# Kernel optimization log

Measured on AMD Instinct MI355X. Metric: run time of the kernel, lower is better.

## Reference

```python
import jax, jax.numpy as jnp
import numpy as np


def setup_inputs() -> dict:
    key = jax.random.key(0)
    ks = jax.random.split(key, 9)
    B, C, H, W = 16, 64, 64, 64
    s = 0.02
    return {
        "x": jax.random.normal(ks[0], (B, C, H, W), dtype=jnp.float32),
        "qw": jax.random.normal(ks[1], (C, C), dtype=jnp.float32) * s,
        "qb": jax.random.normal(ks[2], (C,), dtype=jnp.float32) * s,
        "kw": jax.random.normal(ks[3], (C, C), dtype=jnp.float32) * s,
        "kb": jax.random.normal(ks[4], (C,), dtype=jnp.float32) * s,
        "vw": jax.random.normal(ks[5], (C, C), dtype=jnp.float32) * s,
        "vb": jax.random.normal(ks[6], (C,), dtype=jnp.float32) * s,
        "ow": jax.random.normal(ks[7], (C, C), dtype=jnp.float32) * s,
        "ob": jax.random.normal(ks[8], (C,), dtype=jnp.float32) * s,
    }


def reference(x, qw, qb, kw, kb, vw, vb, ow, ob):
    # x: [B, C, H, W]; 1x1 convs == per-pixel linear maps with weight [out_ch, in_ch]
    B, C, H, W = x.shape
    S = H * W
    xt = x.reshape(B, C, S).transpose(0, 2, 1)  # [B, S, C] tokens over spatial positions
    Q = jnp.einsum("bsc,oc->bso", xt, qw) + qb
    K = jnp.einsum("bsc,oc->bso", xt, kw) + kb
    V = jnp.einsum("bsc,oc->bso", xt, vw) + vb
    scale = 1.0 / jnp.sqrt(jnp.asarray(C, dtype=x.dtype))
    scores = jnp.einsum("bqc,bkc->bqk", Q, K) * scale  # [B, S, S]
    attn = jax.nn.softmax(scores, axis=-1)
    out = jnp.einsum("bqk,bkc->bqc", attn, V)  # [B, S, C]
    out = jnp.einsum("bsc,oc->bso", out, ow) + ob  # out 1x1 conv
    return out.transpose(0, 2, 1).reshape(B, C, H, W)
```

## Files before the change

kernel.cpp:

```cpp
#include <hip/hip_runtime.h>
#include <stdint.h>

#define SS 4096
#define CC 64
#define BB 16

typedef unsigned short u16;
typedef __attribute__((ext_vector_type(8))) __bf16 bf16x8;
typedef __attribute__((ext_vector_type(8))) short short8;
typedef __attribute__((ext_vector_type(4))) short s16x4;
typedef __attribute__((ext_vector_type(4))) float f32x4;

__device__ __forceinline__ uint32_t pkbf(float a, float b) {
    uint32_t ua = __float_as_uint(a) + 0x8000u;
    uint32_t ub = __float_as_uint(b) + 0x8000u;
    return __builtin_amdgcn_perm(ub, ua, 0x07060302u);
}

__device__ __forceinline__ uint32_t cvtpk(float a, float b) {
    uint32_t r;
    asm("v_cvt_pk_bf16_f32 %0, %1, %2" : "=v"(r) : "v"(a), "v"(b));
    return r;
}

__device__ __forceinline__ bf16x8 ldw8(const float* p) {
    f32x4 lo = *(const f32x4*)(p);
    f32x4 hi = *(const f32x4*)(p + 4);
    union { uint32_t u[4]; bf16x8 v; } r;
    r.u[0] = pkbf(lo[0], lo[1]);
    r.u[1] = pkbf(lo[2], lo[3]);
    r.u[2] = pkbf(hi[0], hi[1]);
    r.u[3] = pkbf(hi[2], hi[3]);
    return r.v;
}

__global__ __launch_bounds__(256, 4) void qkv_kernel(
    const float* __restrict__ x,
    const float* __restrict__ qw, const float* __restrict__ qb,
    const float* __restrict__ kw, const float* __restrict__ kb,
    const float* __restrict__ vw, const float* __restrict__ vb,
    u16* __restrict__ Q, u16* __restrict__ K, u16* __restrict__ VT)
{
    const int b    = blockIdx.x & 15;
    const int s0   = (blockIdx.x >> 4) << 6;
    const int tid  = threadIdx.x;
    const int w    = tid >> 6;
    const int lane = tid & 63;
    const int lq   = lane & 15;
    const int quad = lane >> 4;

    __shared__ u16 wt[3][64 * 72];
    __shared__ u16 xt[64 * 72];

    for (int m = 0; m < 3; ++m) {
        const float* wsrc = (m == 0) ? qw : ((m == 1) ? kw : vw);
#pragma unroll
        for (int i = 0; i < 8; ++i) {
            int p  = tid + (i << 8);
            int o  = p >> 5;
            int cp = p & 31;
            const float* wp = wsrc + o * 64 + cp * 2;
            ((uint32_t*)&wt[m][o * 72])[cp] = pkbf(wp[0], wp[1]);
        }
    }
    {
        const int sl = tid & 63;
        const int g  = tid >> 6;
        const float* xp = x + (size_t)b * CC * SS + s0 + sl;
#pragma unroll
        for (int i = 0; i < 8; ++i) {
            int p = g + (i << 2);
            float f0 = xp[(size_t)(2 * p) * SS];
            float f1 = xp[(size_t)(2 * p + 1) * SS];
            ((uint32_t*)&xt[sl * 72])[p] = pkbf(f0, f1);
        }
    }
    __syncthreads();

    bf16x8 a0 = *(const bf16x8*)&xt[(w * 16 + lq) * 72 + quad * 8];
    bf16x8 a1 = *(const bf16x8*)&xt[(w * 16 + lq) * 72 + 32 + quad * 8];
    __syncthreads();

    u16* bb = xt + w * (16 * 72);

    const float QSCALE = 0.125f * 1.44269504088896340736f;

    for (int m = 0; m < 3; ++m) {
        const float* bsrc = (m == 0) ? qb : ((m == 1) ? kb : vb);
        bf16x8 bfr[2][4];
#pragma unroll
        for (int kc = 0; kc < 2; ++kc)
#pragma unroll
            for (int nt = 0; nt < 4; ++nt)
                bfr[kc][nt] = *(const bf16x8*)&wt[m][(nt * 16 + lq) * 72 + kc * 32 + quad * 8];

        f32x4 acc[4];
#pragma unroll
        for (int nt = 0; nt < 4; ++nt) {
            float bv = bsrc[nt * 16 + lq];
            acc[nt] = (f32x4){bv, bv, bv, bv};
        }
#pragma unroll
        for (int nt = 0; nt < 4; ++nt) {
            acc[nt] = __builtin_amdgcn_mfma_f32_16x16x32_bf16(a0, bfr[0][nt], acc[nt], 0, 0, 0);
            acc[nt] = __builtin_amdgcn_mfma_f32_16x16x32_bf16(a1, bfr[1][nt], acc[nt], 0, 0, 0);
        }

        if (m == 2) {
#pragma unroll
            for (int nt = 0; nt < 4; ++nt) {
                int c = nt * 16 + lq;
                uint2 pv;
                pv.x = pkbf(acc[nt][0], acc[nt][1]);
                pv.y = pkbf(acc[nt][2], acc[nt][3]);
                *(uint2*)(VT + ((size_t)(b * CC + c)) * SS + s0 + w * 16 + quad * 4) = pv;
            }
        } else {
            const float scl = (m == 0) ? QSCALE : 1.0f;
#pragma unroll
            for (int nt = 0; nt < 4; ++nt)
#pragma unroll
                for (int r = 0; r < 4; ++r)
                    bb[(quad * 4 + r) * 72 + nt * 16 + lq] =
                        (u16)((__float_as_uint(acc[nt][r] * scl) + 0x8000u) >> 16);

            const int row = lane >> 2;
            const int ch  = (lane & 3) << 4;
            short8 v0 = *(const short8*)&bb[row * 72 + ch];
            short8 v1 = *(const short8*)&bb[row * 72 + ch + 8];
            u16* dst = ((m == 0) ? Q : K) + ((size_t)(b * SS + s0 + w * 16 + row)) * CC + ch;
            *(short8*)dst = v0;
            *(short8*)(dst + 8) = v1;
        }
    }
}

__global__ __launch_bounds__(256, 2) void flash_kernel(
    const u16* __restrict__ Q, const u16* __restrict__ K,
    const u16* __restrict__ Vt, const float* __restrict__ ow,
    const float* __restrict__ ob, float* __restrict__ out)
{
    const int b    = blockIdx.x & 15;
    const int q0   = (blockIdx.x >> 4) << 7;
    const int tid  = threadIdx.x;
    const int w    = tid >> 6;
    const int lane = tid & 63;
    const int lq   = lane & 15;
    const int quad = lane >> 4;

    __shared__ u16 lds_k[2][64 * 64];
    __shared__ u16 lds_v[2][64 * 64];
    __shared__ u16 lds_p[8][16 * 64];

    bf16x8 qf[2][2];
#pragma unroll
    for (int g = 0; g < 2; ++g) {
        const u16* qp = Q + ((size_t)(b * SS + q0 + g * 64 + w * 16 + lq)) * CC + quad * 8;
        qf[g][0] = *(const bf16x8*)(qp);
        qf[g][1] = *(const bf16x8*)(qp + 32);
    }

    f32x4 ot[2][4];
#pragma unroll
    for (int g = 0; g < 2; ++g)
#pragma unroll
        for (int ct = 0; ct < 4; ++ct) ot[g][ct] = (f32x4){0.f, 0.f, 0.f, 0.f};
    float lp[2][4] = {{0.f, 0.f, 0.f, 0.f}, {0.f, 0.f, 0.f, 0.f}};

    const f32x4 ZV = (f32x4){0.f, 0.f, 0.f, 0.f};

    const int srow = tid >> 2;
    const int a    = tid & 3;
    const u16* kg = K + ((size_t)(b * SS + srow)) * CC + a * 16;
    const u16* vg = Vt + ((size_t)(b * CC + srow)) * SS + a * 16;
    const int ssw = srow & 7;
    const int sw0 = srow * 64 + ((((a << 1)    ) ^ ssw) << 3);
    const int sw1 = srow * 64 + ((((a << 1) | 1) ^ ssw) << 3);
    const int kcs = (a >> 1) << 2;
    const int us  = (a & 1) << 2;
    const int vw0 = srow * 64 + (((kcs + 0) ^ ssw) << 3) + us;
    const int vw1 = srow * 64 + (((kcs + 1) ^ ssw) << 3) + us;
    const int vw2 = srow * 64 + (((kcs + 2) ^ ssw) << 3) + us;
    const int vw3 = srow * 64 + (((kcs + 3) ^ ssw) << 3) + us;

    {
        short8 k0 = *(const short8*)(kg);
        short8 k1 = *(const short8*)(kg + 8);
        union { short8 v; s16x4 h[2]; } v0, v1;
        v0.v = *(const short8*)(vg);
        v1.v = *(const short8*)(vg + 8);
        *(short8*)&lds_k[0][sw0] = k0;
        *(short8*)&lds_k[0][sw1] = k1;
        *(s16x4*)&lds_v[0][vw0] = v0.h[0];
        *(s16x4*)&lds_v[0][vw1] = v0.h[1];
        *(s16x4*)&lds_v[0][vw2] = v1.h[0];
        *(s16x4*)&lds_v[0][vw3] = v1.h[1];
    }

    const int lsw = lq & 7;
    u16* pw0 = lds_p[(w << 1)];
    u16* pw1 = lds_p[(w << 1) | 1];

    for (int kt = 0; kt < 64; ++kt) {
        __syncthreads();
        const int buf = kt & 1;

        const int ktn = (kt + 1) & 63;
        const u16* kgn = kg + (size_t)ktn * (64 * CC);
        const u16* vgn = vg + ktn * 64;
        short8 nk0 = *(const short8*)(kgn);
        short8 nk1 = *(const short8*)(kgn + 8);
        union { short8 v; s16x4 h[2]; } nv0, nv1;
        nv0.v = *(const short8*)(vgn);
        nv1.v = *(const short8*)(vgn + 8);

        bf16x8 kf[2][4];
#pragma unroll
        for (int kc = 0; kc < 2; ++kc)
#pragma unroll
            for (int mt = 0; mt < 4; ++mt)
                kf[kc][mt] = *(const bf16x8*)
                    &lds_k[buf][(mt * 16 + lq) * 64 + (((kc << 2) + quad) ^ lsw) * 8];

        f32x4 sa[2][4];
        __builtin_amdgcn_s_setprio(1);
#pragma unroll
        for (int g = 0; g < 2; ++g)
#pragma unroll
            for (int mt = 0; mt < 4; ++mt) {
                sa[g][mt] = __builtin_amdgcn_mfma_f32_16x16x32_bf16(
                    kf[0][mt], qf[g][0], ZV, 0, 0, 0);
                sa[g][mt] = __builtin_amdgcn_mfma_f32_16x16x32_bf16(
                    kf[1][mt], qf[g][1], sa[g][mt], 0, 0, 0);
            }
        __builtin_amdgcn_s_setprio(0);

        bf16x8 vf[2][4];
#pragma unroll
        for (int kc = 0; kc < 2; ++kc)
#pragma unroll
            for (int ct = 0; ct < 4; ++ct)
                vf[kc][ct] = *(const bf16x8*)
                    &lds_v[buf][(ct * 16 + lq) * 64 + (((kc << 2) + quad) ^ lsw) * 8];

#pragma unroll
        for (int g = 0; g < 2; ++g) {
            union { uint32_t u[4]; bf16x8 v; } pf[2];
#pragma unroll
            for (int mt = 0; mt < 4; ++mt) {
                float p0 = __builtin_amdgcn_exp2f(sa[g][mt][0]);
                float p1 = __builtin_amdgcn_exp2f(sa[g][mt][1]);
                float p2 = __builtin_amdgcn_exp2f(sa[g][mt][2]);
                float p3 = __builtin_amdgcn_exp2f(sa[g][mt][3]);
                lp[g][0] += p0; lp[g][1] += p1; lp[g][2] += p2; lp[g][3] += p3;
                pf[mt >> 1].u[(mt & 1) * 2 + 0] = cvtpk(p0, p1);
                pf[mt >> 1].u[(mt & 1) * 2 + 1] = cvtpk(p2, p3);
            }
            __builtin_amdgcn_s_setprio(1);
#pragma unroll
            for (int kc = 0; kc < 2; ++kc)
#pragma unroll
                for (int ct = 0; ct < 4; ++ct)
                    ot[g][ct] = __builtin_amdgcn_mfma_f32_16x16x32_bf16(
                        vf[kc][ct], pf[kc].v, ot[g][ct], 0, 0, 0);
            __builtin_amdgcn_s_setprio(0);
        }

        u16* lkd = lds_k[buf ^ 1];
        u16* lvd = lds_v[buf ^ 1];
        *(short8*)&lkd[sw0] = nk0;
        *(short8*)&lkd[sw1] = nk1;
        *(s16x4*)&lvd[vw0] = nv0.h[0];
        *(s16x4*)&lvd[vw1] = nv0.h[1];
        *(s16x4*)&lvd[vw2] = nv1.h[0];
        *(s16x4*)&lvd[vw3] = nv1.h[1];
    }

    bf16x8 wf[2][4];
#pragma unroll
    for (int kc = 0; kc < 2; ++kc)
#pragma unroll
        for (int nt = 0; nt < 4; ++nt)
            wf[kc][nt] = ldw8(ow + (nt * 16 + lq) * 64 + kc * 32 + quad * 8);
    float bias[4];
#pragma unroll
    for (int nt = 0; nt < 4; ++nt) bias[nt] = ob[nt * 16 + lq];

#pragma unroll
    for (int g = 0; g < 2; ++g) {
        float l = (lp[g][0] + lp[g][1]) + (lp[g][2] + lp[g][3]);
        l += __shfl_xor(l, 16);
        l += __shfl_xor(l, 32);
        const float inv = 1.0f / l;

        u16* po = g ? pw1 : pw0;
#pragma unroll
        for (int ct = 0; ct < 4; ++ct) {
            uint2 pv;
            pv.x = pkbf(ot[g][ct][0] * inv, ot[g][ct][1] * inv);
            pv.y = pkbf(ot[g][ct][2] * inv, ot[g][ct][3] * inv);
            *(uint2*)&po[lq * 64 + (((ct * 2 + (quad >> 1)) ^ lsw) << 3) + (quad & 1) * 4] = pv;
        }
        bf16x8 oa0 = *(const bf16x8*)&po[lq * 64 + (((0 * 4 + quad) ^ lsw) << 3)];
        bf16x8 oa1 = *(const bf16x8*)&po[lq * 64 + (((1 * 4 + quad) ^ lsw) << 3)];

        f32x4 acc[4];
#pragma unroll
        for (int nt = 0; nt < 4; ++nt)
            acc[nt] = (f32x4){bias[nt], bias[nt], bias[nt], bias[nt]};
#pragma unroll
        for (int nt = 0; nt < 4; ++nt) {
            acc[nt] = __builtin_amdgcn_mfma_f32_16x16x32_bf16(oa0, wf[0][nt], acc[nt], 0, 0, 0);
            acc[nt] = __builtin_amdgcn_mfma_f32_16x16x32_bf16(oa1, wf[1][nt], acc[nt], 0, 0, 0);
        }
#pragma unroll
        for (int nt = 0; nt < 4; ++nt) {
            float* dst = out + ((size_t)(b * CC + nt * 16 + lq)) * SS
                       + q0 + g * 64 + w * 16 + quad * 4;
            *(f32x4*)dst = acc[nt];
        }
    }
}

extern "C" void kernel_launch(void* const* d_in, const int* in_sizes, int n_in,
                              void* d_out, int out_size, void* d_ws, size_t ws_size,
                              hipStream_t stream)
{
    const float* x  = (const float*)d_in[0];
    const float* qw = (const float*)d_in[1];
    const float* qb = (const float*)d_in[2];
    const float* kw = (const float*)d_in[3];
    const float* kb = (const float*)d_in[4];
    const float* vw = (const float*)d_in[5];
    const float* vb = (const float*)d_in[6];
    const float* ow = (const float*)d_in[7];
    const float* ob = (const float*)d_in[8];
    float* out = (float*)d_out;

    const size_t T = (size_t)BB * SS * CC;
    u16* Q  = (u16*)d_ws;
    u16* K  = Q + T;
    u16* VT = K + T;

    qkv_kernel<<<dim3(BB * 64), dim3(256), 0, stream>>>(x, qw, qb, kw, kb, vw, vb, Q, K, VT);
    flash_kernel<<<dim3(BB * 32), dim3(256), 0, stream>>>(Q, K, VT, ow, ob, out);
}
```

Measured before the change: 163.1 us.

## Double query rows per flash block and interleave QK and PV per group

```diff
diff --git a/kernel.cpp b/kernel.cpp
--- a/kernel.cpp
+++ b/kernel.cpp
@@ -135,13 +135,13 @@
     }
 }
 
-__global__ __launch_bounds__(256, 2) void flash_kernel(
+__global__ __launch_bounds__(256, 1) void flash_kernel(
     const u16* __restrict__ Q, const u16* __restrict__ K,
     const u16* __restrict__ Vt, const float* __restrict__ ow,
     const float* __restrict__ ob, float* __restrict__ out)
 {
     const int b    = blockIdx.x & 15;
-    const int q0   = (blockIdx.x >> 4) << 7;
+    const int q0   = (blockIdx.x >> 4) << 8;
     const int tid  = threadIdx.x;
     const int w    = tid >> 6;
     const int lane = tid & 63;
@@ -150,22 +150,26 @@
 
     __shared__ u16 lds_k[2][64 * 64];
     __shared__ u16 lds_v[2][64 * 64];
-    __shared__ u16 lds_p[8][16 * 64];
-
-    bf16x8 qf[2][2];
-#pragma unroll
-    for (int g = 0; g < 2; ++g) {
-        const u16* qp = Q + ((size_t)(b * SS + q0 + g * 64 + w * 16 + lq)) * CC + quad * 8;
+    __shared__ u16 lds_p[4][1024];
+
+    bf16x8 qf[4][2];
+#pragma unroll
+    for (int g = 0; g < 4; ++g) {
+        const u16* qp = Q + ((size_t)(b * SS + q0 + w * 64 + g * 16 + lq)) * CC + quad * 8;
         qf[g][0] = *(const bf16x8*)(qp);
         qf[g][1] = *(const bf16x8*)(qp + 32);
     }
 
-    f32x4 ot[2][4];
-#pragma unroll
-    for (int g = 0; g < 2; ++g)
+    f32x4 ot[4][4];
+#pragma unroll
+    for (int g = 0; g < 4; ++g)
 #pragma unroll
         for (int ct = 0; ct < 4; ++ct) ot[g][ct] = (f32x4){0.f, 0.f, 0.f, 0.f};
-    float lp[2][4] = {{0.f, 0.f, 0.f, 0.f}, {0.f, 0.f, 0.f, 0.f}};
+    float lp[4][4];
+#pragma unroll
+    for (int g = 0; g < 4; ++g)
+#pragma unroll
+        for (int r = 0; r < 4; ++r) lp[g][r] = 0.f;
 
     const f32x4 ZV = (f32x4){0.f, 0.f, 0.f, 0.f};
 
@@ -198,8 +202,6 @@
     }
 
     const int lsw = lq & 7;
-    u16* pw0 = lds_p[(w << 1)];
-    u16* pw1 = lds_p[(w << 1) | 1];
 
     for (int kt = 0; kt < 64; ++kt) {
         __syncthreads();
@@ -221,20 +223,6 @@
             for (int mt = 0; mt < 4; ++mt)
                 kf[kc][mt] = *(const bf16x8*)
                     &lds_k[buf][(mt * 16 + lq) * 64 + (((kc << 2) + quad) ^ lsw) * 8];
-
-        f32x4 sa[2][4];
-        __builtin_amdgcn_s_setprio(1);
-#pragma unroll
-        for (int g = 0; g < 2; ++g)
-#pragma unroll
-            for (int mt = 0; mt < 4; ++mt) {
-                sa[g][mt] = __builtin_amdgcn_mfma_f32_16x16x32_bf16(
-                    kf[0][mt], qf[g][0], ZV, 0, 0, 0);
-                sa[g][mt] = __builtin_amdgcn_mfma_f32_16x16x32_bf16(
-                    kf[1][mt], qf[g][1], sa[g][mt], 0, 0, 0);
-            }
-        __builtin_amdgcn_s_setprio(0);
-
         bf16x8 vf[2][4];
 #pragma unroll
         for (int kc = 0; kc < 2; ++kc)
@@ -244,18 +232,30 @@
                     &lds_v[buf][(ct * 16 + lq) * 64 + (((kc << 2) + quad) ^ lsw) * 8];
 
 #pragma unroll
-        for (int g = 0; g < 2; ++g) {
+        for (int g = 0; g < 4; ++g) {
+            f32x4 sa[4];
+            __builtin_amdgcn_s_setprio(1);
+#pragma unroll
+            for (int mt = 0; mt < 4; ++mt) {
+                sa[mt] = __builtin_amdgcn_mfma_f32_16x16x32_bf16(
+                    kf[0][mt], qf[g][0], ZV, 0, 0, 0);
+                sa[mt] = __builtin_amdgcn_mfma_f32_16x16x32_bf16(
+                    kf[1][mt], qf[g][1], sa[mt], 0, 0, 0);
+            }
+            __builtin_amdgcn_s_setprio(0);
+
             union { uint32_t u[4]; bf16x8 v; } pf[2];
 #pragma unroll
             for (int mt = 0; mt < 4; ++mt) {
-                float p0 = __builtin_amdgcn_exp2f(sa[g][mt][0]);
-                float p1 = __builtin_amdgcn_exp2f(sa[g][mt][1]);
-                float p2 = __builtin_amdgcn_exp2f(sa[g][mt][2]);
-                float p3 = __builtin_amdgcn_exp2f(sa[g][mt][3]);
+                float p0 = __builtin_amdgcn_exp2f(sa[mt][0]);
+                float p1 = __builtin_amdgcn_exp2f(sa[mt][1]);
+                float p2 = __builtin_amdgcn_exp2f(sa[mt][2]);
+                float p3 = __builtin_amdgcn_exp2f(sa[mt][3]);
                 lp[g][0] += p0; lp[g][1] += p1; lp[g][2] += p2; lp[g][3] += p3;
                 pf[mt >> 1].u[(mt & 1) * 2 + 0] = cvtpk(p0, p1);
                 pf[mt >> 1].u[(mt & 1) * 2 + 1] = cvtpk(p2, p3);
             }
+
             __builtin_amdgcn_s_setprio(1);
 #pragma unroll
             for (int kc = 0; kc < 2; ++kc)
@@ -286,14 +286,15 @@
 #pragma unroll
     for (int nt = 0; nt < 4; ++nt) bias[nt] = ob[nt * 16 + lq];
 
-#pragma unroll
-    for (int g = 0; g < 2; ++g) {
+    u16* po = lds_p[w];
+
+#pragma unroll
+    for (int g = 0; g < 4; ++g) {
         float l = (lp[g][0] + lp[g][1]) + (lp[g][2] + lp[g][3]);
         l += __shfl_xor(l, 16);
         l += __shfl_xor(l, 32);
         const float inv = 1.0f / l;
 
-        u16* po = g ? pw1 : pw0;
 #pragma unroll
         for (int ct = 0; ct < 4; ++ct) {
             uint2 pv;
@@ -316,7 +317,7 @@
 #pragma unroll
         for (int nt = 0; nt < 4; ++nt) {
             float* dst = out + ((size_t)(b * CC + nt * 16 + lq)) * SS
-                       + q0 + g * 64 + w * 16 + quad * 4;
+                       + q0 + w * 64 + g * 16 + quad * 4;
             *(f32x4*)dst = acc[nt];
         }
     }
@@ -343,5 +344,5 @@
     u16* VT = K + T;
 
     qkv_kernel<<<dim3(BB * 64), dim3(256), 0, stream>>>(x, qw, qb, kw, kb, vw, vb, Q, K, VT);
-    flash_kernel<<<dim3(BB * 32), dim3(256), 0, stream>>>(Q, K, VT, ow, ob, out);
-}
+    flash_kernel<<<dim3(BB * 16), dim3(256), 0, stream>>>(Q, K, VT, ow, ob, out);
+}
```

After: 185.1 us. 1.13x slower.

## Process two KV tiles per barrier with quad-buffered LDS staging

Applied to the files above, without the earlier changes.

```diff
diff --git a/kernel.cpp b/kernel.cpp
--- a/kernel.cpp
+++ b/kernel.cpp
@@ -148,9 +148,9 @@
     const int lq   = lane & 15;
     const int quad = lane >> 4;
 
-    __shared__ u16 lds_k[2][64 * 64];
-    __shared__ u16 lds_v[2][64 * 64];
-    __shared__ u16 lds_p[8][16 * 64];
+    __shared__ u16 lds_k[4][64 * 64];
+    __shared__ u16 lds_v[4][64 * 64];
+    __shared__ u16 lds_p[4][1024];
 
     bf16x8 qf[2][2];
 #pragma unroll
@@ -183,98 +183,119 @@
     const int vw2 = srow * 64 + (((kcs + 2) ^ ssw) << 3) + us;
     const int vw3 = srow * 64 + (((kcs + 3) ^ ssw) << 3) + us;
 
+#define STAGE(BUF, K0_, K1_, V0_, V1_) do {                                   \
+    *(short8*)&lds_k[BUF][sw0] = K0_;                                         \
+    *(short8*)&lds_k[BUF][sw1] = K1_;                                         \
+    *(s16x4*)&lds_v[BUF][vw0] = V0_.h[0];                                     \
+    *(s16x4*)&lds_v[BUF][vw1] = V0_.h[1];                                     \
+    *(s16x4*)&lds_v[BUF][vw2] = V1_.h[0];                                     \
+    *(s16x4*)&lds_v[BUF][vw3] = V1_.h[1];                                     \
+} while (0)
+
     {
-        short8 k0 = *(const short8*)(kg);
-        short8 k1 = *(const short8*)(kg + 8);
-        union { short8 v; s16x4 h[2]; } v0, v1;
-        v0.v = *(const short8*)(vg);
-        v1.v = *(const short8*)(vg + 8);
-        *(short8*)&lds_k[0][sw0] = k0;
-        *(short8*)&lds_k[0][sw1] = k1;
-        *(s16x4*)&lds_v[0][vw0] = v0.h[0];
-        *(s16x4*)&lds_v[0][vw1] = v0.h[1];
-        *(s16x4*)&lds_v[0][vw2] = v1.h[0];
-        *(s16x4*)&lds_v[0][vw3] = v1.h[1];
+        short8 k0a = *(const short8*)(kg);
+        short8 k1a = *(const short8*)(kg + 8);
+        union { short8 v; s16x4 h[2]; } v0a, v1a;
+        v0a.v = *(const short8*)(vg);
+        v1a.v = *(const short8*)(vg + 8);
+        const u16* kg1 = kg + (size_t)(64 * CC);
+        const u16* vg1 = vg + 64;
+        short8 k0b = *(const short8*)(kg1);
+        short8 k1b = *(const short8*)(kg1 + 8);
+        union { short8 v; s16x4 h[2]; } v0b, v1b;
+        v0b.v = *(const short8*)(vg1);
+        v1b.v = *(const short8*)(vg1 + 8);
+        STAGE(0, k0a, k1a, v0a, v1a);
+        STAGE(1, k0b, k1b, v0b, v1b);
     }
 
     const int lsw = lq & 7;
-    u16* pw0 = lds_p[(w << 1)];
-    u16* pw1 = lds_p[(w << 1) | 1];
-
-    for (int kt = 0; kt < 64; ++kt) {
+
+#define SUBTILE(BUF) do {                                                     \
+    bf16x8 kf[2][4];                                                          \
+    _Pragma("unroll")                                                         \
+    for (int kc = 0; kc < 2; ++kc)                                            \
+        _Pragma("unroll")                                                     \
+        for (int mt = 0; mt < 4; ++mt)                                        \
+            kf[kc][mt] = *(const bf16x8*)                                     \
+                &lds_k[BUF][(mt * 16 + lq) * 64 + (((kc << 2) + quad) ^ lsw) * 8]; \
+    f32x4 sa[2][4];                                                           \
+    __builtin_amdgcn_s_setprio(1);                                            \
+    _Pragma("unroll")                                                         \
+    for (int g = 0; g < 2; ++g)                                               \
+        _Pragma("unroll")                                                     \
+        for (int mt = 0; mt < 4; ++mt) {                                      \
+            sa[g][mt] = __builtin_amdgcn_mfma_f32_16x16x32_bf16(              \
+                kf[0][mt], qf[g][0], ZV, 0, 0, 0);                            \
+            sa[g][mt] = __builtin_amdgcn_mfma_f32_16x16x32_bf16(              \
+                kf[1][mt], qf[g][1], sa[g][mt], 0, 0, 0);                     \
+        }                                                                     \
+    __builtin_amdgcn_s_setprio(0);                                            \
+    bf16x8 vf[2][4];                                                          \
+    _Pragma("unroll")                                                         \
+    for (int kc = 0; kc < 2; ++kc)                                            \
+        _Pragma("unroll")                                                     \
+        for (int ct = 0; ct < 4; ++ct)                                        \
+            vf[kc][ct] = *(const bf16x8*)                                     \
+                &lds_v[BUF][(ct * 16 + lq) * 64 + (((kc << 2) + quad) ^ lsw) * 8]; \
+    _Pragma("unroll")                                                         \
+    for (int g = 0; g < 2; ++g) {                                             \
+        union { uint32_t u[4]; bf16x8 v; } pf[2];                             \
+        _Pragma("unroll")                                                     \
+        for (int mt = 0; mt < 4; ++mt) {                                      \
+            float p0 = __builtin_amdgcn_exp2f(sa[g][mt][0]);                  \
+            float p1 = __builtin_amdgcn_exp2f(sa[g][mt][1]);                  \
+            float p2 = __builtin_amdgcn_exp2f(sa[g][mt][2]);                  \
+            float p3 = __builtin_amdgcn_exp2f(sa[g][mt][3]);                  \
+            lp[g][0] += p0; lp[g][1] += p1; lp[g][2] += p2; lp[g][3] += p3;   \
+            pf[mt >> 1].u[(mt & 1) * 2 + 0] = cvtpk(p0, p1);                  \
+            pf[mt >> 1].u[(mt & 1) * 2 + 1] = cvtpk(p2, p3);                  \
+        }                                                                     \
+        __builtin_amdgcn_s_setprio(1);                                        \
+        _Pragma("unroll")                                                     \
+        for (int kc = 0; kc < 2; ++kc)                                        \
+            _Pragma("unroll")                                                 \
+            for (int ct = 0; ct < 4; ++ct)                                    \
+                ot[g][ct] = __builtin_amdgcn_mfma_f32_16x16x32_bf16(          \
+                    vf[kc][ct], pf[kc].v, ot[g][ct], 0, 0, 0);                \
+        __builtin_amdgcn_s_setprio(0);                                        \
+    }                                                                         \
+} while (0)
+
+    for (int it = 0; it < 32; ++it) {
         __syncthreads();
-        const int buf = kt & 1;
-
-        const int ktn = (kt + 1) & 63;
-        const u16* kgn = kg + (size_t)ktn * (64 * CC);
-        const u16* vgn = vg + ktn * 64;
-        short8 nk0 = *(const short8*)(kgn);
-        short8 nk1 = *(const short8*)(kgn + 8);
-        union { short8 v; s16x4 h[2]; } nv0, nv1;
-        nv0.v = *(const short8*)(vgn);
-        nv1.v = *(const short8*)(vgn + 8);
-
-        bf16x8 kf[2][4];
-#pragma unroll
-        for (int kc = 0; kc < 2; ++kc)
-#pragma unroll
-            for (int mt = 0; mt < 4; ++mt)
-                kf[kc][mt] = *(const bf16x8*)
-                    &lds_k[buf][(mt * 16 + lq) * 64 + (((kc << 2) + quad) ^ lsw) * 8];
-
-        f32x4 sa[2][4];
-        __builtin_amdgcn_s_setprio(1);
-#pragma unroll
-        for (int g = 0; g < 2; ++g)
-#pragma unroll
-            for (int mt = 0; mt < 4; ++mt) {
-                sa[g][mt] = __builtin_amdgcn_mfma_f32_16x16x32_bf16(
-                    kf[0][mt], qf[g][0], ZV, 0, 0, 0);
-                sa[g][mt] = __builtin_amdgcn_mfma_f32_16x16x32_bf16(
-                    kf[1][mt], qf[g][1], sa[g][mt], 0, 0, 0);
-            }
-        __builtin_amdgcn_s_setprio(0);
-
-        bf16x8 vf[2][4];
-#pragma unroll
-        for (int kc = 0; kc < 2; ++kc)
-#pragma unroll
-            for (int ct = 0; ct < 4; ++ct)
-                vf[kc][ct] = *(const bf16x8*)
-                    &lds_v[buf][(ct * 16 + lq) * 64 + (((kc << 2) + quad) ^ lsw) * 8];
-
-#pragma unroll
-        for (int g = 0; g < 2; ++g) {
-            union { uint32_t u[4]; bf16x8 v; } pf[2];
-#pragma unroll
-            for (int mt = 0; mt < 4; ++mt) {
-                float p0 = __builtin_amdgcn_exp2f(sa[g][mt][0]);
-                float p1 = __builtin_amdgcn_exp2f(sa[g][mt][1]);
-                float p2 = __builtin_amdgcn_exp2f(sa[g][mt][2]);
-                float p3 = __builtin_amdgcn_exp2f(sa[g][mt][3]);
-                lp[g][0] += p0; lp[g][1] += p1; lp[g][2] += p2; lp[g][3] += p3;
-                pf[mt >> 1].u[(mt & 1) * 2 + 0] = cvtpk(p0, p1);
-                pf[mt >> 1].u[(mt & 1) * 2 + 1] = cvtpk(p2, p3);
-            }
-            __builtin_amdgcn_s_setprio(1);
-#pragma unroll
-            for (int kc = 0; kc < 2; ++kc)
-#pragma unroll
-                for (int ct = 0; ct < 4; ++ct)
-                    ot[g][ct] = __builtin_amdgcn_mfma_f32_16x16x32_bf16(
-                        vf[kc][ct], pf[kc].v, ot[g][ct], 0, 0, 0);
-            __builtin_amdgcn_s_setprio(0);
-        }
-
-        u16* lkd = lds_k[buf ^ 1];
-        u16* lvd = lds_v[buf ^ 1];
-        *(short8*)&lkd[sw0] = nk0;
-        *(short8*)&lkd[sw1] = nk1;
-        *(s16x4*)&lvd[vw0] = nv0.h[0];
-        *(s16x4*)&lvd[vw1] = nv0.h[1];
-        *(s16x4*)&lvd[vw2] = nv1.h[0];
-        *(s16x4*)&lvd[vw3] = nv1.h[1];
-    }
+        const int pr = it & 1;
+
+        const int kt0 = (2 * it + 2) & 63;
+        const int kt1 = (2 * it + 3) & 63;
+        const u16* kga = kg + (size_t)kt0 * (64 * CC);
+        const u16* vga = vg + kt0 * 64;
+        const u16* kgb = kg + (size_t)kt1 * (64 * CC);
+        const u16* vgb = vg + kt1 * 64;
+        short8 nk0a = *(const short8*)(kga);
+        short8 nk1a = *(const short8*)(kga + 8);
+        union { short8 v; s16x4 h[2]; } nv0a, nv1a;
+        nv0a.v = *(const short8*)(vga);
+        nv1a.v = *(const short8*)(vga + 8);
+        short8 nk0b = *(const short8*)(kgb);
+        short8 nk1b = *(const short8*)(kgb + 8);
+        union { short8 v; s16x4 h[2]; } nv0b, nv1b;
+        nv0b.v = *(const short8*)(vgb);
+        nv1b.v = *(const short8*)(vgb + 8);
+
+        if (pr == 0) { SUBTILE(0); SUBTILE(1); }
+        else         { SUBTILE(2); SUBTILE(3); }
+
+        if (pr == 0) {
+            STAGE(2, nk0a, nk1a, nv0a, nv1a);
+            STAGE(3, nk0b, nk1b, nv0b, nv1b);
+        } else {
+            STAGE(0, nk0a, nk1a, nv0a, nv1a);
+            STAGE(1, nk0b, nk1b, nv0b, nv1b);
+        }
+    }
+#undef SUBTILE
+#undef STAGE
 
     bf16x8 wf[2][4];
 #pragma unroll
@@ -285,6 +306,8 @@
     float bias[4];
 #pragma unroll
     for (int nt = 0; nt < 4; ++nt) bias[nt] = ob[nt * 16 + lq];
+
+    u16* po = lds_p[w];
 
 #pragma unroll
     for (int g = 0; g < 2; ++g) {
@@ -293,7 +316,6 @@
         l += __shfl_xor(l, 32);
         const float inv = 1.0f / l;
 
-        u16* po = g ? pw1 : pw0;
 #pragma unroll
         for (int ct = 0; ct < 4; ++ct) {
             uint2 pv;
```

Measured after the change: 165.5 us. No clear change (+1.5%).
